# Kernel optimization log

Measured on AMD Instinct MI355X. Metric: run time of the kernel, lower is better.

Reference implementation:

```python
import jax, jax.numpy as jnp
import numpy as np

K = 10  # knn neighbors
EPS = 1e-5  # BatchNorm eps


def mish(x):
    # x * tanh(softplus(x)), numerically stable softplus
    return x * jnp.tanh(jnp.logaddexp(x, 0.0))


def bn(x, g, b, m, v, nd):
    # inference-mode BatchNorm over channel axis 1
    shp = (1, -1) + (1,) * (nd - 2)
    scale = g.reshape(shp) / jnp.sqrt(v.reshape(shp) + EPS)
    return (x - m.reshape(shp)) * scale + b.reshape(shp)


def graph_feature(x, k):
    # x: [B, C, N] -> edge features [B, 2C, N, k]
    xt = jnp.swapaxes(x, 1, 2)  # [B, N, C]
    sq = jnp.sum(x * x, axis=1)  # [B, N]
    # negative squared pairwise distance [B, N, N]
    neg = 2.0 * jnp.einsum('bcn,bcm->bnm', x, x) - sq[:, :, None] - sq[:, None, :]
    idx = jax.lax.top_k(neg, k)[1]  # [B, N, k] nearest-neighbor indices
    nbr = jax.vmap(lambda a, i: a[i])(xt, idx)  # [B, N, k, C]
    ctr = jnp.broadcast_to(xt[:, :, None, :], nbr.shape)
    feat = jnp.concatenate([nbr - ctr, ctr], axis=-1)  # [B, N, k, 2C]
    return jnp.transpose(feat, (0, 3, 1, 2))  # [B, 2C, N, k]


def c2(w, x):  # 1x1 Conv2d
    return jnp.einsum('oc,bcnk->bonk', w, x)


def c1(w, x):  # 1x1 Conv1d
    return jnp.einsum('oc,bcn->bon', w, x)


def setup_inputs() -> dict:
    key = jax.random.key(0)
    ks = jax.random.split(key, 32)
    B, d, N = 8, 3, 2048
    emb, nb = 1024, 6
    def w(k_, o, c):
        return jax.random.normal(k_, (o, c), dtype=jnp.float32) * (1.0 / np.sqrt(c))
    inp = {
        'x': jax.random.normal(ks[0], (B, d, N), dtype=jnp.float32),
        'w1': w(ks[1], 64, 2 * d), 'w2': w(ks[2], 64, 64),
        'w3': w(ks[3], 64, 128), 'w4': w(ks[4], 64, 64),
        'w5': w(ks[5], 64, 128), 'w6': w(ks[6], emb, 192),
        'w7': w(ks[7], 512, emb + 192), 'w8': w(ks[8], 256, 512),
        'w9': w(ks[9], d * nb, 256),
        'g15': jax.random.uniform(ks[10], (5, 64), jnp.float32, 0.5, 1.5),
        'b15': jax.random.normal(ks[11], (5, 64), jnp.float32) * 0.1,
        'm15': jax.random.normal(ks[12], (5, 64), jnp.float32) * 0.1,
        'v15': jax.random.uniform(ks[13], (5, 64), jnp.float32, 0.5, 1.5),
        'g6': jax.random.uniform(ks[14], (emb,), jnp.float32, 0.5, 1.5),
        'b6': jax.random.normal(ks[15], (emb,), jnp.float32) * 0.1,
        'm6': jax.random.normal(ks[16], (emb,), jnp.float32) * 0.1,
        'v6': jax.random.uniform(ks[17], (emb,), jnp.float32, 0.5, 1.5),
        'g7': jax.random.uniform(ks[18], (512,), jnp.float32, 0.5, 1.5),
        'b7': jax.random.normal(ks[19], (512,), jnp.float32) * 0.1,
        'm7': jax.random.normal(ks[20], (512,), jnp.float32) * 0.1,
        'v7': jax.random.uniform(ks[21], (512,), jnp.float32, 0.5, 1.5),
        'g8': jax.random.uniform(ks[22], (256,), jnp.float32, 0.5, 1.5),
        'b8': jax.random.normal(ks[23], (256,), jnp.float32) * 0.1,
        'm8': jax.random.normal(ks[24], (256,), jnp.float32) * 0.1,
        'v8': jax.random.uniform(ks[25], (256,), jnp.float32, 0.5, 1.5),
    }
    return inp


def reference(x, w1, w2, w3, w4, w5, w6, w7, w8, w9,
              g15, b15, m15, v15, g6, b6, m6, v6,
              g7, b7, m7, v7, g8, b8, m8, v8):
    N = x.shape[2]
    f = graph_feature(x, K)                                   # [B, 6, N, K]
    h = mish(bn(c2(w1, f), g15[0], b15[0], m15[0], v15[0], 4))
    h = mish(bn(c2(w2, h), g15[1], b15[1], m15[1], v15[1], 4))
    x1 = jnp.max(h, axis=-1)                                  # [B, 64, N]
    f = graph_feature(x1, K)
    h = mish(bn(c2(w3, f), g15[2], b15[2], m15[2], v15[2], 4))
    h = mish(bn(c2(w4, h), g15[3], b15[3], m15[3], v15[3], 4))
    x2 = jnp.max(h, axis=-1)
    f = graph_feature(x2, K)
    h = mish(bn(c2(w5, f), g15[4], b15[4], m15[4], v15[4], 4))
    x3 = jnp.max(h, axis=-1)
    cat = jnp.concatenate([x1, x2, x3], axis=1)               # [B, 192, N]
    h6 = mish(bn(c1(w6, cat), g6, b6, m6, v6, 3))             # [B, emb, N]
    glob = jnp.max(h6, axis=-1, keepdims=True)
    glob = jnp.broadcast_to(glob, (glob.shape[0], glob.shape[1], N))
    h = jnp.concatenate([glob, cat], axis=1)                  # [B, emb+192, N]
    h = mish(bn(c1(w7, h), g7, b7, m7, v7, 3))
    h = mish(bn(c1(w8, h), g8, b8, m8, v8, 3))
    return c1(w9, h)                                          # [B, 18, N]
```

## Files before the change

### kernel.cpp

```cpp
#include <hip/hip_runtime.h>
#include <math.h>

#define BN_EPS 1e-5f
typedef unsigned long long u64;
typedef __attribute__((ext_vector_type(8))) short bf16x8;
typedef __attribute__((ext_vector_type(8))) unsigned short u16x8;
typedef __attribute__((ext_vector_type(4))) float f32x4;

__device__ __forceinline__ float mishf(float x){
  float u = __expf(fminf(x, 20.f));
  float w = u * (u + 2.f);
  return x * w / (w + 2.f);
}

__device__ __forceinline__ unsigned fenc(float f){
  unsigned u = __float_as_uint(f);
  return u ^ ((unsigned)((int)u >> 31) | 0x80000000u);
}
__device__ __forceinline__ float fdec(unsigned e){
  unsigned u = (e & 0x80000000u) ? (e & 0x7fffffffu) : ~e;
  return __uint_as_float(u);
}

__device__ __forceinline__ void bfsplit(float a, unsigned short &h, unsigned short &l){
  unsigned u = __float_as_uint(a);
  unsigned hb = (u + 0x7FFFu + ((u >> 16) & 1u)) >> 16;
  h = (unsigned short)hb;
  float hf = __uint_as_float(hb << 16);
  float r = a - hf;
  unsigned v = __float_as_uint(r);
  l = (unsigned short)((v + 0x7FFFu + ((v >> 16) & 1u)) >> 16);
}

__device__ __forceinline__ u64 mkkey(float v, int i){
  return ((u64)fenc(v) << 32) | (unsigned)(~i);
}
__device__ __forceinline__ int keyidx(u64 k){ return (int)(~(unsigned)k); }

__device__ __forceinline__ void ins10k(u64 (&L)[10], u64 k){
  if (k <= L[9]) return;
  #pragma unroll
  for (int p = 9; p >= 1; --p)
    L[p] = (k > L[p-1]) ? L[p-1] : ((k > L[p]) ? k : L[p]);
  L[0] = (k > L[0]) ? k : L[0];
}

__device__ __forceinline__ void ins10s(unsigned (&S)[10], unsigned e){
  #pragma unroll
  for (int p = 9; p >= 1; --p){
    unsigned ns;
    asm("v_med3_u32 %0, %1, %2, %3" : "=v"(ns) : "v"(e), "v"(S[p-1]), "v"(S[p]));
    S[p] = ns;
  }
  S[0] = (e > S[0]) ? e : S[0];
}

#define TOPK_INIT(S, I, eth) do { \
  _Pragma("unroll") \
  for (int _j = 0; _j < 10; ++_j) { S[_j] = 0x007FFFFFu; I[_j] = 0x7fffffffu; } \
  eth = 0x007FFFFFu; } while (0)

__device__ __forceinline__ void topk_push32(unsigned (&S)[10], unsigned (&I)[10],
                                            unsigned &eth, float v, unsigned i){
  unsigned e = fenc(v);
  if (e > eth) {
    #pragma unroll
    for (int p = 9; p >= 1; --p) {
      bool gp = e > S[p-1];
      bool gc = e > S[p];
      I[p] = gp ? I[p-1] : (gc ? i : I[p]);
      unsigned ns;
      asm("v_med3_u32 %0, %1, %2, %3" : "=v"(ns) : "v"(e), "v"(S[p-1]), "v"(S[p]));
      S[p] = ns;
    }
    bool g0 = e > S[0];
    I[0] = g0 ? i : I[0];
    S[0] = g0 ? e : S[0];
    eth = S[9];
  }
}
#define KSENT mkkey(-INFINITY, 0x7fffffff)

__global__ void k_diag(float* __restrict__ out, float v){ out[0] = v; }

__global__ __launch_bounds__(256)
void k_zero(unsigned* __restrict__ p){
  p[blockIdx.x * 256 + threadIdx.x] = 0u;
}

__global__ __launch_bounds__(256)
void k_knn3(const float* __restrict__ x, int* __restrict__ idxout){
  __shared__ __align__(16) char smem[33024];
  float4* pts4   = (float4*)smem;
  unsigned* m1u  = (unsigned*)smem;
  unsigned* m2u  = (unsigned*)(smem + 10240);
  unsigned* thr  = (unsigned*)(smem + 12800);
  int*      cnt  = (int*)(smem + 12864);
  u64*      buf  = (u64*)(smem + 12928);
  const int t  = threadIdx.x;
  const int b  = blockIdx.x >> 7;
  const int p0 = (blockIdx.x & 127) * 16;
  const int pt = t & 15, ch = t >> 4;
  const float* xb = x + (size_t)b * 6144;

  for (int i = t; i < 2048; i += 256) {
    float x0 = xb[i], x1 = xb[2048 + i], x2 = xb[4096 + i];
    float s2 = x0 * x0; s2 = fmaf(x1, x1, s2); s2 = fmaf(x2, x2, s2);
    pts4[(i >> 7) * 129 + (i & 127)] = make_float4(x0, x1, x2, s2);
  }
  __syncthreads();

  const int g = p0 + pt;
  const float4 ov = pts4[(g >> 7) * 129 + (g & 127)];
  unsigned S[10];
  #pragma unroll
  for (int j = 0; j < 10; ++j) S[j] = 0x007FFFFFu;
  const float4* cp = pts4 + ch * 129;
  #pragma unroll 4
  for (int j = 0; j < 128; ++j) {
    float4 pv = cp[j];
    float dot = ov.x * pv.x; dot = fmaf(ov.y, pv.y, dot); dot = fmaf(ov.z, pv.z, dot);
    float key = fmaf(2.f, dot, -ov.w) - pv.w;
    ins10s(S, fenc(key));
  }
  __syncthreads();

  #pragma unroll
  for (int j = 0; j < 10; ++j)
    m1u[(ch * 10 + j) * 16 + pt] = S[j];
  __syncthreads();

  if (t < 64) {
    int p1 = t >> 2, q = t & 3;
    unsigned F[10];
    #pragma unroll
    for (int j = 0; j < 10; ++j) F[j] = 0x007FFFFFu;
    for (int c2 = 0; c2 < 4; ++c2)
      #pragma unroll
      for (int j = 0; j < 10; ++j)
        ins10s(F, m1u[((q * 4 + c2) * 10 + j) * 16 + p1]);
    #pragma unroll
    for (int j = 0; j < 10; ++j)
      m2u[(q * 10 + j) * 16 + p1] = F[j];
  }
  __syncthreads();

  if (t < 16) {
    unsigned F[10];
    #pragma unroll
    for (int j = 0; j < 10; ++j) F[j] = 0x007FFFFFu;
    for (int q = 0; q < 4; ++q)
      #pragma unroll
      for (int j = 0; j < 10; ++j)
        ins10s(F, m2u[(q * 10 + j) * 16 + t]);
    thr[t] = F[9];
    cnt[t] = 0;
  }
  __syncthreads();

  const unsigned th = thr[pt];
  for (int j = 0; j < 128; ++j) {
    int c = ch * 128 + j;
    float x0 = xb[c], x1 = xb[2048 + c], x2 = xb[4096 + c];
    float s2 = x0 * x0; s2 = fmaf(x1, x1, s2); s2 = fmaf(x2, x2, s2);
    float dot = ov.x * x0; dot = fmaf(ov.y, x1, dot); dot = fmaf(ov.z, x2, dot);
    float key = fmaf(2.f, dot, -ov.w) - s2;
    unsigned e = fenc(key);
    if (e >= th) {
      int slot = atomicAdd(&cnt[pt], 1);
      if (slot < 16) buf[pt * 16 + slot] = ((u64)e << 32) | (unsigned)(~c);
    }
  }
  __syncthreads();

  if (t < 16) {
    u64 F[10];
    #pragma unroll
    for (int j = 0; j < 10; ++j) F[j] = KSENT;
    int n = cnt[t]; n = (n < 16) ? n : 16;
    for (int e2 = 0; e2 < n; ++e2) ins10k(F, buf[t * 16 + e2]);
    #pragma unroll
    for (int j = 0; j < 10; ++j)
      idxout[(size_t)(b * 2048 + p0 + t) * 10 + j] = keyidx(F[j]);
  }
}

__global__ __launch_bounds__(256)
void k_knn2p(const unsigned short* __restrict__ H, const unsigned short* __restrict__ Lp,
             const float* __restrict__ sq, u64* __restrict__ pk){
  __shared__ __align__(16) char smem[20480];
  float* ssB = (float*)smem;
  u64*   mg  = (u64*)smem;

  const int t  = threadIdx.x;
  const int bx = blockIdx.x;
  const int cc = bx & 7;
  const int rg = (bx >> 3) & 31;
  const int b  = bx >> 8;
  const int p0 = rg * 64;
  const int c0 = cc * 256;
  const int lane = t & 63, w = t >> 6;
  const int la  = (lane & 15) * 8;
  const int sub = lane >> 4;
  const int qrow = w * 16 + (lane & 15);
  const int rt = t % 10;

  const size_t ag = ((size_t)((b * 2048 + p0) >> 4) + w) * 8 + sub;
  bf16x8 aH0 = *(const bf16x8*)&H [ ag      * 128 + la];
  bf16x8 aL0 = *(const bf16x8*)&Lp[ ag      * 128 + la];
  bf16x8 aH1 = *(const bf16x8*)&H [(ag + 4) * 128 + la];
  bf16x8 aL1 = *(const bf16x8*)&Lp[(ag + 4) * 128 + la];

  ssB[t] = sq[b * 2048 + c0 + (t & 255)];
  const float nsA = -sq[b * 2048 + p0 + qrow];

  unsigned S[10], I[10], eth;
  TOPK_INIT(S, I, eth);
  __syncthreads();

  for (int m0 = 0; m0 < 256; m0 += 64) {
    const size_t cgb = ((size_t)((b * 2048 + c0 + m0) >> 4)) * 8 + sub;
    #pragma unroll
    for (int tile = 0; tile < 4; ++tile) {
      const size_t cg = (cgb + (size_t)tile * 8) * 128 + la;
      bf16x8 bH0 = *(const bf16x8*)&H [cg];
      bf16x8 bL0 = *(const bf16x8*)&Lp[cg];
      bf16x8 bH1 = *(const bf16x8*)&H [cg + 512];
      bf16x8 bL1 = *(const bf16x8*)&Lp[cg + 512];
      f32x4 acc = {0.f, 0.f, 0.f, 0.f};
      acc = __builtin_amdgcn_mfma_f32_16x16x32_bf16(bH0, aL0, acc, 0, 0, 0);
      acc = __builtin_amdgcn_mfma_f32_16x16x32_bf16(bL0, aH0, acc, 0, 0, 0);
      acc = __builtin_amdgcn_mfma_f32_16x16x32_bf16(bH0, aH0, acc, 0, 0, 0);
      acc = __builtin_amdgcn_mfma_f32_16x16x32_bf16(bH1, aL1, acc, 0, 0, 0);
      acc = __builtin_amdgcn_mfma_f32_16x16x32_bf16(bL1, aH1, acc, 0, 0, 0);
      acc = __builtin_amdgcn_mfma_f32_16x16x32_bf16(bH1, aH1, acc, 0, 0, 0);
      float4 s4 = *(const float4*)&ssB[m0 + tile * 16 + sub * 4];
      int cbase = c0 + m0 + tile * 16 + sub * 4;
      topk_push32(S, I, eth, fmaf(2.f, acc[0], nsA) - s4.x, cbase);
      topk_push32(S, I, eth, fmaf(2.f, acc[1], nsA) - s4.y, cbase + 1);
      topk_push32(S, I, eth, fmaf(2.f, acc[2], nsA) - s4.z, cbase + 2);
      topk_push32(S, I, eth, fmaf(2.f, acc[3], nsA) - s4.w, cbase + 3);
    }
  }
  __syncthreads();

  #pragma unroll
  for (int j = 0; j < 10; ++j) {
    int rj = j + rt; rj = (rj >= 10) ? rj - 10 : rj;
    mg[(qrow * 4 + sub) * 10 + rj] = ((u64)S[j] << 32) | (unsigned)(~I[j]);
  }
  __syncthreads();
  if (t < 64) {
    u64 F[10];
    #pragma unroll
    for (int j = 0; j < 10; ++j) F[j] = KSENT;
    for (int c2 = 0; c2 < 4; ++c2)
      #pragma unroll
      for (int j = 0; j < 10; ++j) {
        int rj = j + rt; rj = (rj >= 10) ? rj - 10 : rj;
        ins10k(F, mg[(t * 4 + c2) * 10 + rj]);
      }
    size_t base = (size_t)(b * 2048 + p0 + t) * 80 + cc * 10;
    #pragma unroll
    for (int j = 0; j < 10; ++j) pk[base + j] = F[j];
  }
}

__global__ __launch_bounds__(64)
void k_kmerge(const u64* __restrict__ pk, int* __restrict__ idxout){
  int row = blockIdx.x * 64 + threadIdx.x;
  u64 F[10];
  #pragma unroll
  for (int j = 0; j < 10; ++j) F[j] = KSENT;
  size_t base = (size_t)row * 80;
  for (int e = 0; e < 80; ++e) ins10k(F, pk[base + e]);
  #pragma unroll
  for (int j = 0; j < 10; ++j) idxout[(size_t)row * 10 + j] = keyidx(F[j]);
}

__global__ __launch_bounds__(256)
void k_uv3(const float* __restrict__ x, const float* __restrict__ w1,
           const float* __restrict__ gg, const float* __restrict__ vv,
           float* __restrict__ UV){
  int i = blockIdx.x * 256 + threadIdx.x;
  int p = i >> 6, o = i & 63;
  int b = p >> 11, n = p & 2047;
  float s = gg[o] / sqrtf(vv[o] + BN_EPS);
  const float* xb = x + (size_t)b * 6144 + n;
  float x0 = xb[0], x1 = xb[2048], x2 = xb[4096];
  const float* wr = w1 + o * 6;
  float u = s * (wr[0] * x0 + wr[1] * x1 + wr[2] * x2);
  float v = s * ((wr[3] - wr[0]) * x0 + (wr[4] - wr[1]) * x1 + (wr[5] - wr[2]) * x2);
  UV[(size_t)p * 128 + o] = u;
  UV[(size_t)p * 128 + 64 + o] = v;
}

__global__ __launch_bounds__(256)
void k_uv(const float* __restrict__ A, int lda, int aoff,
          const float* __restrict__ w,
          const float* __restrict__ gg, const float* __restrict__ vv,
          float* __restrict__ UV){
  __shared__ float As[16][68];
  __shared__ float Bs[16][68];
  __shared__ float ss[64];
  const int t = threadIdx.x;
  const int tx = t & 15, ty = t >> 4;
  const int m0 = blockIdx.x * 64;
  const int half = blockIdx.y;
  if (t < 64) ss[t] = gg[t] / sqrtf(vv[t] + BN_EPS);
  __syncthreads();
  float acc[4][4] = {};
  for (int k0 = 0; k0 < 64; k0 += 16) {
    for (int i = t; i < 1024; i += 256) {
      int m = i >> 4, k = i & 15;
      As[k][m] = A[(size_t)(m0 + m) * lda + aoff + k0 + k];
    }
    for (int i = t; i < 1024; i += 256) {
      int n = i >> 4, k = i & 15;
      int kk = k0 + k;
      float wv = half ? (w[n * 128 + 64 + kk] - w[n * 128 + kk]) : w[n * 128 + kk];
      Bs[k][n] = wv * ss[n];
    }
    __syncthreads();
    #pragma unroll
    for (int k = 0; k < 16; ++k) {
      float4 a4 = *(const float4*)&As[k][tx * 4];
      float4 b4 = *(const float4*)&Bs[k][ty * 4];
      float am[4] = {a4.x, a4.y, a4.z, a4.w};
      float bm[4] = {b4.x, b4.y, b4.z, b4.w};
      #pragma unroll
      for (int q = 0; q < 4; ++q)
        #pragma unroll
        for (int r = 0; r < 4; ++r)
          acc[q][r] = fmaf(am[q], bm[r], acc[q][r]);
    }
    __syncthreads();
  }
  #pragma unroll
  for (int q = 0; q < 4; ++q)
    #pragma unroll
    for (int r = 0; r < 4; ++r)
      UV[(size_t)(m0 + tx * 4 + q) * 128 + half * 64 + ty * 4 + r] = acc[q][r];
}

__global__ __launch_bounds__(256)
void k_edge2(const float* __restrict__ UV, const int* __restrict__ idx,
             const float* __restrict__ w2,
             const float* __restrict__ g1, const float* __restrict__ b1,
             const float* __restrict__ m1, const float* __restrict__ v1,
             const float* __restrict__ g2, const float* __restrict__ b2,
             const float* __restrict__ m2, const float* __restrict__ v2,
             float* __restrict__ cat, int coff,
             unsigned short* __restrict__ kH, unsigned short* __restrict__ kL,
             float* __restrict__ sqout){
  __shared__ float Ha[64][81];
  __shared__ float Ws[64][68];
  __shared__ float o1s[64], s2s[64], o2s[64];
  __shared__ int   ejs[80];
  const int t = threadIdx.x;
  const int p0 = blockIdx.x * 8;
  const int batch = p0 >> 11;
  if (t < 80) ejs[t] = batch * 2048 + (idx[p0 * 10 + t] & 2047);
  if (t < 64) {
    float s1 = g1[t] / sqrtf(v1[t] + BN_EPS);
    o1s[t] = b1[t] - m1[t] * s1;
    float s2 = g2[t] / sqrtf(v2[t] + BN_EPS);
    s2s[t] = s2;
    o2s[t] = b2[t] - m2[t] * s2;
  }
  for (int i = t; i < 4096; i += 256) {
    int k = i & 63, n = i >> 6;
    Ws[k][n] = w2[n * 64 + k];
  }
  __syncthreads();

  for (int i = t; i < 5120; i += 256) {
    int e = i >> 6, c = i & 63;
    int p = p0 + e / 10;
    float hv = UV[(size_t)ejs[e] * 128 + c] + UV[(size_t)p * 128 + 64 + c] + o1s[c];
    Ha[c][e] = mishf(hv);
  }
  __syncthreads();

  const int tx = t & 15, ty = t >> 4;
  float acc[5][4] = {};
  #pragma unroll 8
  for (int k = 0; k < 64; ++k) {
    float av[5];
    #pragma unroll
    for (int i2 = 0; i2 < 5; ++i2) av[i2] = Ha[k][tx * 5 + i2];
    float4 b4 = *(const float4*)&Ws[k][ty * 4];
    float bv[4] = {b4.x, b4.y, b4.z, b4.w};
    #pragma unroll
    for (int i2 = 0; i2 < 5; ++i2)
      #pragma unroll
      for (int r = 0; r < 4; ++r)
        acc[i2][r] = fmaf(av[i2], bv[r], acc[i2][r]);
  }
  __syncthreads();
  #pragma unroll
  for (int i2 = 0; i2 < 5; ++i2)
    #pragma unroll
    for (int r = 0; r < 4; ++r) {
      int o = ty * 4 + r;
      Ha[o][tx * 5 + i2] = mishf(acc[i2][r] * s2s[o] + o2s[o]);
    }
  __syncthreads();

  for (int i = t; i < 512; i += 256) {
    int p = i >> 6, o = i & 63;
    float mx = Ha[o][p * 10];
    #pragma unroll
    for (int k = 1; k < 10; ++k) mx = fmaxf(mx, Ha[o][p * 10 + k]);
    cat[(size_t)(p0 + p) * 192 + coff + o] = mx;
    unsigned short hh, ll;
    bfsplit(mx, hh, ll);
    int n = p0 + p;
    size_t pos = ((size_t)(n >> 4) * 8 + (o >> 3)) * 128 + (n & 15) * 8 + (o & 7);
    kH[pos] = hh; kL[pos] = ll;
    float r = mx * mx;
    #pragma unroll
    for (int m = 32; m; m >>= 1) r += __shfl_xor(r, m);
    if (o == 0) sqout[p0 + p] = r;
  }
}

__global__ __launch_bounds__(256)
void k_edge3(const float* __restrict__ UV, const int* __restrict__ idx,
             const float* __restrict__ gg, const float* __restrict__ bb,
             const float* __restrict__ mn, const float* __restrict__ vv,
             float* __restrict__ cat){
  int i = blockIdx.x * 256 + threadIdx.x;
  int p = i >> 6, o = i & 63;
  int batch = p >> 11;
  float s = gg[o] / sqrtf(vv[o] + BN_EPS);
  float of = bb[o] - mn[o] * s;
  float v_ = UV[(size_t)p * 128 + 64 + o] + of;
  float mx = -INFINITY;
  #pragma unroll
  for (int k = 0; k < 10; ++k) {
    int j = batch * 2048 + (idx[p * 10 + k] & 2047);
    mx = fmaxf(mx, mishf(UV[(size_t)j * 128 + o] + v_));
  }
  cat[(size_t)p * 192 + 128 + o] = mx;
}

__global__ __launch_bounds__(256)
void k_split(const float* __restrict__ src, int ld, int koff, int K,
             unsigned short* __restrict__ H, unsigned short* __restrict__ L){
  int i = blockIdx.x * 256 + threadIdx.x;
  int kg = K >> 3;
  int n = i / kg, g = i - n * kg;
  const float* s = &src[(size_t)n * ld + koff + g * 8];
  float4 v0 = *(const float4*)s, v1 = *(const float4*)(s + 4);
  float vv[8] = {v0.x, v0.y, v0.z, v0.w, v1.x, v1.y, v1.z, v1.w};
  u16x8 hh, ll;
  #pragma unroll
  for (int q = 0; q < 8; ++q) {
    unsigned short h_, l_;
    bfsplit(vv[q], h_, l_);
    hh[q] = h_; ll[q] = l_;
  }
  size_t pos = ((size_t)(n >> 4) * kg + g) * 128 + (n & 15) * 8;
  *(u16x8*)&H[pos] = hh;
  *(u16x8*)&L[pos] = ll;
}

#define EP_BNMISH      0
#define EP_MAXGLOB     1
#define EP_BIAS_BNMISH 2

template<int EPI>
__global__ __launch_bounds__(256)
void k_gemm(const unsigned short* __restrict__ APH, const unsigned short* __restrict__ APL,
            const unsigned short* __restrict__ WPH, const unsigned short* __restrict__ WPL,
            int K,
            const float* __restrict__ gg, const float* __restrict__ bb,
            const float* __restrict__ mn, const float* __restrict__ vv,
            const float* __restrict__ bias,
            float* __restrict__ out, int ldo,
            unsigned short* __restrict__ oH, unsigned short* __restrict__ oL, int oldo,
            unsigned* __restrict__ glob)
{
  __shared__ float red[64][17];
  const int t = threadIdx.x;
  const int lane = t & 63, w = t >> 6;
  const int m0 = blockIdx.x * 64, n0 = blockIdx.y * 64;
  const int kg = K >> 3;
  const int la = (lane & 15) * 8;
  f32x4 acc[4] = {{0,0,0,0},{0,0,0,0},{0,0,0,0},{0,0,0,0}};
  const size_t abase = ((size_t)((m0 >> 4) + w) * kg + (lane >> 4)) * 128 + la;

  for (int k0 = 0; k0 < K; k0 += 32) {
    size_t ao = abase + (size_t)(k0 >> 3) * 128;
    bf16x8 aH = *(const bf16x8*)&APH[ao];
    bf16x8 aL = *(const bf16x8*)&APL[ao];
    #pragma unroll
    for (int tt = 0; tt < 4; ++tt) {
      size_t wo = ((size_t)((n0 >> 4) + tt) * kg + (k0 >> 3) + (lane >> 4)) * 128 + la;
      bf16x8 bH = *(const bf16x8*)&WPH[wo];
      bf16x8 bL = *(const bf16x8*)&WPL[wo];
      acc[tt] = __builtin_amdgcn_mfma_f32_16x16x32_bf16(aL, bH, acc[tt], 0, 0, 0);
      acc[tt] = __builtin_amdgcn_mfma_f32_16x16x32_bf16(aH, bL, acc[tt], 0, 0, 0);
      acc[tt] = __builtin_amdgcn_mfma_f32_16x16x32_bf16(aH, bH, acc[tt], 0, 0, 0);
    }
  }

  const int mrow = m0 + w * 16 + ((lane >> 4) << 2);
  const int batch = m0 >> 11;

  if (EPI == EP_MAXGLOB) {
    #pragma unroll
    for (int tt = 0; tt < 4; ++tt) {
      int nn = n0 + tt * 16 + (lane & 15);
      float s = gg[nn] / sqrtf(vv[nn] + BN_EPS);
      float f = bb[nn] - mn[nn] * s;
      float mx = -INFINITY;
      #pragma unroll
      for (int r = 0; r < 4; ++r) mx = fmaxf(mx, mishf(acc[tt][r] * s + f));
      red[tt * 16 + (lane & 15)][w * 4 + (lane >> 4)] = mx;
    }
    __syncthreads();
    if (t < 64) {
      float v = red[t][0];
      #pragma unroll
      for (int q = 1; q < 16; ++q) v = fmaxf(v, red[t][q]);
      atomicMax(&glob[batch * 1024 + n0 + t], fenc(v));
    }
  } else {
    #pragma unroll
    for (int tt = 0; tt < 4; ++tt) {
      int nn = n0 + tt * 16 + (lane & 15);
      float s = gg[nn] / sqrtf(vv[nn] + BN_EPS);
      float f = bb[nn] - mn[nn] * s;
      float bv = (EPI == EP_BIAS_BNMISH) ? bias[batch * 512 + nn] : 0.f;
      #pragma unroll
      for (int r = 0; r < 4; ++r) {
        int m = mrow + r;
        float h = mishf((acc[tt][r] + bv) * s + f);
        if (EPI == EP_BIAS_BNMISH) {
          unsigned short hh, ll;
          bfsplit(h, hh, ll);
          size_t pos = ((size_t)(m >> 4) * (oldo >> 3) + (nn >> 3)) * 128
                       + (m & 15) * 8 + (nn & 7);
          oH[pos] = hh; oL[pos] = ll;
        } else {
          out[(size_t)m * ldo + nn] = h;
        }
      }
    }
  }
}

__global__ __launch_bounds__(256)
void k_t7(const unsigned* __restrict__ glob, const float* __restrict__ w7,
          float* __restrict__ t7){
  int i = blockIdx.x * 256 + threadIdx.x;
  int b = i >> 9, o = i & 511;
  float acc = 0.f;
  for (int c = 0; c < 1024; ++c)
    acc = fmaf(w7[(size_t)o * 1216 + c], fdec(glob[b * 1024 + c]), acc);
  t7[i] = acc;
}

__global__ __launch_bounds__(256)
void k_out(const float* __restrict__ h8, const float* __restrict__ w9,
           float* __restrict__ out)
{
  __shared__ float row[4][256];
  const int t = threadIdx.x;
  const int g = t >> 6, l = t & 63;
  const int p = blockIdx.x * 4 + g;
  for (int c = l; c < 256; c += 64)
    row[g][c] = h8[(size_t)p * 256 + c];
  __syncthreads();
  if (l < 18) {
    float acc = 0.f;
    for (int c = 0; c < 256; ++c)
      acc = fmaf(row[g][c], w9[l * 256 + c], acc);
    int b = p >> 11, n = p & 2047;
    out[(size_t)b * 36864 + l * 2048 + n] = acc;
  }
}

extern "C" void kernel_launch(void* const* d_in, const int* in_sizes, int n_in,
                              void* d_out, int out_size, void* d_ws, size_t ws_size,
                              hipStream_t stream)
{
  const size_t OFF_IDX  = 262144;
  const size_t OFF_CAT  = 917504;
  const size_t OFF_GLOB = 13500416;
  const size_t OFF_T7   = 13533184;
  const size_t OFF_H7   = 13549568;
  const size_t OFF_KNN  = OFF_H7 + 8388608;
  const size_t OFF_H8   = 47104000;
  const size_t NEED     = 63881216;

  static const int EXP[26] = {
    49152, 384, 4096, 8192, 4096, 8192, 196608, 622592, 131072, 4608,
    320, 320, 320, 320, 1024, 1024, 1024, 1024,
    512, 512, 512, 512, 256, 256, 256, 256 };
  if (n_in < 26) { k_diag<<<1,1,0,stream>>>((float*)d_out, 16384.f); return; }
  for (int i = 0; i < 26; ++i)
    if (in_sizes[i] != EXP[i]) {
      k_diag<<<1,1,0,stream>>>((float*)d_out, 4096.f + 128.f * i); return;
    }
  if (out_size != 294912) { k_diag<<<1,1,0,stream>>>((float*)d_out, 20480.f); return; }
  if (ws_size < NEED) {
    k_diag<<<1,1,0,stream>>>((float*)d_out, 24576.f + (float)(ws_size >> 20)); return;
  }

  const float* x  = (const float*)d_in[0];
  const float* w1 = (const float*)d_in[1];
  const float* w2 = (const float*)d_in[2];
  const float* w3 = (const float*)d_in[3];
  const float* w4 = (const float*)d_in[4];
  const float* w5 = (const float*)d_in[5];
  const float* w6 = (const float*)d_in[6];
  const float* w7 = (const float*)d_in[7];
  const float* w8 = (const float*)d_in[8];
  const float* w9 = (const float*)d_in[9];
  const float* g15 = (const float*)d_in[10];
  const float* b15 = (const float*)d_in[11];
  const float* m15 = (const float*)d_in[12];
  const float* v15 = (const float*)d_in[13];
  const float* g6 = (const float*)d_in[14];
  const float* b6 = (const float*)d_in[15];
  const float* m6 = (const float*)d_in[16];
  const float* v6 = (const float*)d_in[17];
  const float* g7 = (const float*)d_in[18];
  const float* b7 = (const float*)d_in[19];
  const float* m7 = (const float*)d_in[20];
  const float* v7 = (const float*)d_in[21];
  const float* g8 = (const float*)d_in[22];
  const float* b8 = (const float*)d_in[23];
  const float* m8 = (const float*)d_in[24];
  const float* v8 = (const float*)d_in[25];

  char* ws = (char*)d_ws;
  int*      idx  = (int*)(ws + OFF_IDX);
  float*    cat  = (float*)(ws + OFF_CAT);
  unsigned* glob = (unsigned*)(ws + OFF_GLOB);
  float*    t7   = (float*)(ws + OFF_T7);
  float*    UV   = (float*)(ws + OFF_H7);
  float*    h8   = (float*)(ws + OFF_H8);
  float*    sq   = (float*)(ws + OFF_H8);
  u64*      pk   = (u64*)(ws + OFF_H8 + 65536);
  unsigned short* knnH = (unsigned short*)(ws + OFF_KNN);
  unsigned short* knnL = (unsigned short*)(ws + OFF_KNN + 2097152);

  unsigned short* catH = (unsigned short*)(ws + OFF_H8);
  unsigned short* catL = (unsigned short*)(ws + OFF_H8 + 6291456);
  unsigned short* h7H  = (unsigned short*)(ws + OFF_H7);
  unsigned short* h7L  = (unsigned short*)(ws + OFF_H7 + 16777216);
  unsigned short* w6H  = (unsigned short*)(ws + OFF_CAT);
  unsigned short* w6L  = (unsigned short*)(ws + OFF_CAT + 393216);
  unsigned short* w7H  = (unsigned short*)(ws + OFF_CAT + 786432);
  unsigned short* w7L  = (unsigned short*)(ws + OFF_CAT + 983040);
  unsigned short* w8H  = (unsigned short*)(ws + OFF_CAT + 1179648);
  unsigned short* w8L  = (unsigned short*)(ws + OFF_CAT + 1441792);

  k_zero<<<32, 256, 0, stream>>>(glob);

  k_knn3<<<1024, 256, 0, stream>>>(x, idx);
  k_uv3<<<4096, 256, 0, stream>>>(x, w1, g15 + 0, v15 + 0, UV);
  k_edge2<<<2048, 256, 0, stream>>>(UV, idx, w2,
      g15 + 0,  b15 + 0,  m15 + 0,  v15 + 0,
      g15 + 64, b15 + 64, m15 + 64, v15 + 64, cat, 0, knnH, knnL, sq);

  k_knn2p<<<2048, 256, 0, stream>>>(knnH, knnL, sq, pk);
  k_kmerge<<<256, 64, 0, stream>>>(pk, idx);
  dim3 guv(256, 2);
  k_uv<<<guv, 256, 0, stream>>>(cat, 192, 0, w3, g15 + 128, v15 + 128, UV);
  k_edge2<<<2048, 256, 0, stream>>>(UV, idx, w4,
      g15 + 128, b15 + 128, m15 + 128, v15 + 128,
      g15 + 192, b15 + 192, m15 + 192, v15 + 192, cat, 64, knnH, knnL, sq);

  k_knn2p<<<2048, 256, 0, stream>>>(knnH, knnL, sq, pk);
  k_kmerge<<<256, 64, 0, stream>>>(pk, idx);
  k_uv<<<guv, 256, 0, stream>>>(cat, 192, 64, w5, g15 + 256, v15 + 256, UV);
  k_edge3<<<4096, 256, 0, stream>>>(UV, idx,
      g15 + 256, b15 + 256, m15 + 256, v15 + 256, cat);

  k_split<<<1536, 256, 0, stream>>>(cat, 192, 0, 192, catH, catL);
  k_split<<<96, 256, 0, stream>>>(w6, 192, 0, 192, w6H, w6L);
  k_split<<<48, 256, 0, stream>>>(w7, 1216, 1024, 192, w7H, w7L);
  k_split<<<64, 256, 0, stream>>>(w8, 512, 0, 512, w8H, w8L);

  dim3 g6g(256, 16);
  k_gemm<EP_MAXGLOB><<<g6g, 256, 0, stream>>>(
      catH, catL, w6H, w6L, 192, g6, b6, m6, v6,
      nullptr, nullptr, 0, nullptr, nullptr, 0, glob);
  k_t7<<<16, 256, 0, stream>>>(glob, w7, t7);
  dim3 g7g(256, 8);
  k_gemm<EP_BIAS_BNMISH><<<g7g, 256, 0, stream>>>(
      catH, catL, w7H, w7L, 192, g7, b7, m7, v7,
      t7, nullptr, 0, h7H, h7L, 512, nullptr);
  dim3 g8g(256, 4);
  k_gemm<EP_BNMISH><<<g8g, 256, 0, stream>>>(
      h7H, h7L, w8H, w8L, 512, g8, b8, m8, v8,
      nullptr, h8, 256, nullptr, nullptr, 0, nullptr);
  k_out<<<4096, 256, 0, stream>>>(h8, w9, (float*)d_out);
}
```

Before: 650.6 us.

## Use two-pass threshold-then-collect top-k in the bf16 split kNN kernel

Replaces per-lane top-10 tracking with indices in k_knn2p by a two-pass scheme. A first pass keeps only value-only top-10 lists using branchless med3 insertion. The four partial lists per row are merged in shared memory to get a per-row threshold. A second pass recomputes the MFMA distances and appends candidates at or above the threshold to a small per-row buffer with shared atomics, and that buffer is then sorted. This removes the divergent index-carrying insertion but doubles the MFMA and global loads, and drops candidates beyond 16 per row when there are ties.

```diff
diff --git a/kernel.cpp b/kernel.cpp
--- a/kernel.cpp
+++ b/kernel.cpp
@@ -53,31 +53,6 @@
     S[p] = ns;
   }
   S[0] = (e > S[0]) ? e : S[0];
-}
-
-#define TOPK_INIT(S, I, eth) do { \
-  _Pragma("unroll") \
-  for (int _j = 0; _j < 10; ++_j) { S[_j] = 0x007FFFFFu; I[_j] = 0x7fffffffu; } \
-  eth = 0x007FFFFFu; } while (0)
-
-__device__ __forceinline__ void topk_push32(unsigned (&S)[10], unsigned (&I)[10],
-                                            unsigned &eth, float v, unsigned i){
-  unsigned e = fenc(v);
-  if (e > eth) {
-    #pragma unroll
-    for (int p = 9; p >= 1; --p) {
-      bool gp = e > S[p-1];
-      bool gc = e > S[p];
-      I[p] = gp ? I[p-1] : (gc ? i : I[p]);
-      unsigned ns;
-      asm("v_med3_u32 %0, %1, %2, %3" : "=v"(ns) : "v"(e), "v"(S[p-1]), "v"(S[p]));
-      S[p] = ns;
-    }
-    bool g0 = e > S[0];
-    I[0] = g0 ? i : I[0];
-    S[0] = g0 ? e : S[0];
-    eth = S[9];
-  }
 }
 #define KSENT mkkey(-INFINITY, 0x7fffffff)
 
@@ -189,8 +164,11 @@
 void k_knn2p(const unsigned short* __restrict__ H, const unsigned short* __restrict__ Lp,
              const float* __restrict__ sq, u64* __restrict__ pk){
   __shared__ __align__(16) char smem[20480];
-  float* ssB = (float*)smem;
-  u64*   mg  = (u64*)smem;
+  float*    ssB = (float*)smem;
+  unsigned* sc1 = (unsigned*)(smem + 1024);
+  unsigned* th  = (unsigned*)(smem + 11424);
+  int*      cnt = (int*)(smem + 11680);
+  u64*      buf = (u64*)(smem + 11936);
 
   const int t  = threadIdx.x;
   const int bx = blockIdx.x;
@@ -203,7 +181,6 @@
   const int la  = (lane & 15) * 8;
   const int sub = lane >> 4;
   const int qrow = w * 16 + (lane & 15);
-  const int rt = t % 10;
 
   const size_t ag = ((size_t)((b * 2048 + p0) >> 4) + w) * 8 + sub;
   bf16x8 aH0 = *(const bf16x8*)&H [ ag      * 128 + la];
@@ -214,10 +191,54 @@
   ssB[t] = sq[b * 2048 + c0 + (t & 255)];
   const float nsA = -sq[b * 2048 + p0 + qrow];
 
-  unsigned S[10], I[10], eth;
-  TOPK_INIT(S, I, eth);
-  __syncthreads();
-
+  unsigned S[10];
+  #pragma unroll
+  for (int j = 0; j < 10; ++j) S[j] = 0x007FFFFFu;
+  __syncthreads();
+
+  for (int m0 = 0; m0 < 256; m0 += 64) {
+    const size_t cgb = ((size_t)((b * 2048 + c0 + m0) >> 4)) * 8 + sub;
+    #pragma unroll
+    for (int tile = 0; tile < 4; ++tile) {
+      const size_t cg = (cgb + (size_t)tile * 8) * 128 + la;
+      bf16x8 bH0 = *(const bf16x8*)&H [cg];
+      bf16x8 bL0 = *(const bf16x8*)&Lp[cg];
+      bf16x8 bH1 = *(const bf16x8*)&H [cg + 512];
+      bf16x8 bL1 = *(const bf16x8*)&Lp[cg + 512];
+      f32x4 acc = {0.f, 0.f, 0.f, 0.f};
+      acc = __builtin_amdgcn_mfma_f32_16x16x32_bf16(bH0, aL0, acc, 0, 0, 0);
+      acc = __builtin_amdgcn_mfma_f32_16x16x32_bf16(bL0, aH0, acc, 0, 0, 0);
+      acc = __builtin_amdgcn_mfma_f32_16x16x32_bf16(bH0, aH0, acc, 0, 0, 0);
+      acc = __builtin_amdgcn_mfma_f32_16x16x32_bf16(bH1, aL1, acc, 0, 0, 0);
+      acc = __builtin_amdgcn_mfma_f32_16x16x32_bf16(bL1, aH1, acc, 0, 0, 0);
+      acc = __builtin_amdgcn_mfma_f32_16x16x32_bf16(bH1, aH1, acc, 0, 0, 0);
+      float4 s4 = *(const float4*)&ssB[m0 + tile * 16 + sub * 4];
+      ins10s(S, fenc(fmaf(2.f, acc[0], nsA) - s4.x));
+      ins10s(S, fenc(fmaf(2.f, acc[1], nsA) - s4.y));
+      ins10s(S, fenc(fmaf(2.f, acc[2], nsA) - s4.z));
+      ins10s(S, fenc(fmaf(2.f, acc[3], nsA) - s4.w));
+    }
+  }
+
+  #pragma unroll
+  for (int j = 0; j < 10; ++j)
+    sc1[(sub * 10 + j) * 65 + qrow] = S[j];
+  __syncthreads();
+
+  if (t < 64) {
+    unsigned F[10];
+    #pragma unroll
+    for (int j = 0; j < 10; ++j) F[j] = 0x007FFFFFu;
+    for (int s2 = 0; s2 < 4; ++s2)
+      #pragma unroll
+      for (int j = 0; j < 10; ++j)
+        ins10s(F, sc1[(s2 * 10 + j) * 65 + t]);
+    th[t] = F[9];
+    cnt[t] = 0;
+  }
+  __syncthreads();
+
+  const unsigned thq = th[qrow];
   for (int m0 = 0; m0 < 256; m0 += 64) {
     const size_t cgb = ((size_t)((b * 2048 + c0 + m0) >> 4)) * 8 + sub;
     #pragma unroll
@@ -236,30 +257,25 @@
       acc = __builtin_amdgcn_mfma_f32_16x16x32_bf16(bH1, aH1, acc, 0, 0, 0);
       float4 s4 = *(const float4*)&ssB[m0 + tile * 16 + sub * 4];
       int cbase = c0 + m0 + tile * 16 + sub * 4;
-      topk_push32(S, I, eth, fmaf(2.f, acc[0], nsA) - s4.x, cbase);
-      topk_push32(S, I, eth, fmaf(2.f, acc[1], nsA) - s4.y, cbase + 1);
-      topk_push32(S, I, eth, fmaf(2.f, acc[2], nsA) - s4.z, cbase + 2);
-      topk_push32(S, I, eth, fmaf(2.f, acc[3], nsA) - s4.w, cbase + 3);
-    }
-  }
-  __syncthreads();
-
-  #pragma unroll
-  for (int j = 0; j < 10; ++j) {
-    int rj = j + rt; rj = (rj >= 10) ? rj - 10 : rj;
-    mg[(qrow * 4 + sub) * 10 + rj] = ((u64)S[j] << 32) | (unsigned)(~I[j]);
-  }
-  __syncthreads();
+      #pragma unroll
+      for (int r = 0; r < 4; ++r) {
+        float sr = (r == 0) ? s4.x : (r == 1) ? s4.y : (r == 2) ? s4.z : s4.w;
+        unsigned e = fenc(fmaf(2.f, acc[r], nsA) - sr);
+        if (e >= thq) {
+          int slot = atomicAdd(&cnt[qrow], 1);
+          if (slot < 16) buf[qrow * 16 + slot] = ((u64)e << 32) | (unsigned)(~(cbase + r));
+        }
+      }
+    }
+  }
+  __syncthreads();
+
   if (t < 64) {
     u64 F[10];
     #pragma unroll
     for (int j = 0; j < 10; ++j) F[j] = KSENT;
-    for (int c2 = 0; c2 < 4; ++c2)
-      #pragma unroll
-      for (int j = 0; j < 10; ++j) {
-        int rj = j + rt; rj = (rj >= 10) ? rj - 10 : rj;
-        ins10k(F, mg[(t * 4 + c2) * 10 + rj]);
-      }
+    int n = cnt[t]; n = (n < 16) ? n : 16;
+    for (int e2 = 0; e2 < n; ++e2) ins10k(F, buf[t * 16 + e2]);
     size_t base = (size_t)(b * 2048 + p0 + t) * 80 + cc * 10;
     #pragma unroll
     for (int j = 0; j < 10; ++j) pk[base + j] = F[j];
```

Result: faster. 624.8 us (-4.0%).
